# Kernel optimization log

Measured on AMD Instinct MI355X. Metric: run time of the kernel, lower is better.

## Reference

```python
import jax, jax.numpy as jnp
import numpy as np

EMBED_DIM = 1024
NUM_HEADS = 16
HEAD_DIM = EMBED_DIM // NUM_HEADS


def setup_inputs() -> dict:
    key = jax.random.key(0)
    ks = jax.random.split(key, 9)
    B, S, D = 4, 2048, EMBED_DIM
    s = 1.0 / np.sqrt(D)
    inp = {
        "x": jax.random.normal(ks[0], (B, S, D), dtype=jnp.float32),
        "Wq": jax.random.uniform(ks[1], (D, D), jnp.float32, -s, s),
        "bq": jax.random.uniform(ks[2], (D,), jnp.float32, -s, s),
        "Wk": jax.random.uniform(ks[3], (D, D), jnp.float32, -s, s),
        "bk": jax.random.uniform(ks[4], (D,), jnp.float32, -s, s),
        "Wv": jax.random.uniform(ks[5], (D, D), jnp.float32, -s, s),
        "bv": jax.random.uniform(ks[6], (D,), jnp.float32, -s, s),
        "Wo": jax.random.uniform(ks[7], (D, D), jnp.float32, -s, s),
        "bo": jax.random.uniform(ks[8], (D,), jnp.float32, -s, s),
    }
    return inp


def reference(x, Wq, bq, Wk, bk, Wv, bv, Wo, bo):
    B, S, D = x.shape
    H, Hd = NUM_HEADS, HEAD_DIM
    scale = 1.0 / jnp.sqrt(jnp.asarray(Hd, x.dtype))

    def split_heads(t):  # (B,S,D) -> (B,H,S,Hd)
        return t.reshape(B, S, H, Hd).transpose(0, 2, 1, 3)

    q = split_heads(x @ Wq + bq)
    k = split_heads(x @ Wk + bk)
    v = split_heads(x @ Wv + bv)

    scores = jnp.einsum("bhqd,bhkd->bhqk", q, k) * scale
    attn = jax.nn.softmax(scores, axis=-1)  # dropout is identity in eval mode
    out = jnp.einsum("bhqk,bhkd->bhqd", attn, v)
    out = out.transpose(0, 2, 1, 3).reshape(B, S, D)
    return out @ Wo + bo
```

## Files before the change

### kernel.cpp

```cpp
#include <hip/hip_runtime.h>
#include <cstdint>

typedef unsigned short u16;
typedef uint32_t u32;
typedef float f32x4 __attribute__((ext_vector_type(4)));
typedef short s16x8 __attribute__((ext_vector_type(8)));
typedef u16 u16x4 __attribute__((ext_vector_type(4)));
typedef u32 u32x2 __attribute__((ext_vector_type(2)));

__device__ __forceinline__ u16 f2bf(float f) {
  u32 u = __builtin_bit_cast(u32, f);
  u += 0x7FFFu + ((u >> 16) & 1u);
  return (u16)(u >> 16);
}

__device__ __forceinline__ u32 pack2bf(float lo, float hi) {
  return __builtin_amdgcn_perm(__builtin_bit_cast(u32, hi) + 0x8000u,
                               __builtin_bit_cast(u32, lo) + 0x8000u, 0x07060302u);
}

template <typename T>
__device__ __forceinline__ T ldv(const void* p) {
  T v;
  __builtin_memcpy(&v, __builtin_assume_aligned(p, 16), sizeof(T));
  return v;
}

__device__ __forceinline__ void gload_lds16(const void* g, void* l) {
  __builtin_amdgcn_global_load_lds((const __attribute__((address_space(1))) void*)g,
                                   (__attribute__((address_space(3))) void*)l, 16, 0, 0);
}

__global__ __launch_bounds__(256) void cvt_x_k(const float* __restrict__ in,
                                               u16* __restrict__ out) {
  const int i = (blockIdx.x * 256 + threadIdx.x) * 4;
  float4 v = *(const float4*)(in + i);
  u16x4 o;
  o.x = f2bf(v.x); o.y = f2bf(v.y); o.z = f2bf(v.z); o.w = f2bf(v.w);
  *(u16x4*)(out + i) = o;
}

__global__ __launch_bounds__(256) void prep_w_k(const float* __restrict__ Wq,
                                                const float* __restrict__ Wk,
                                                const float* __restrict__ Wv,
                                                const float* __restrict__ Wo,
                                                u16* __restrict__ out) {
  __shared__ u16 t[64][72];
  const float* W = (blockIdx.z == 0) ? Wq : (blockIdx.z == 1) ? Wk
                  : (blockIdx.z == 2) ? Wv : Wo;
  u16* O = out + (size_t)blockIdx.z * 1024 * 1024;
  const int n0 = blockIdx.x * 64, k0 = blockIdx.y * 64;
  const int tid = threadIdx.x;
#pragma unroll
  for (int i = 0; i < 16; ++i) {
    int e = i * 256 + tid;
    int r = e >> 6, c = e & 63;
    t[r][c] = f2bf(W[(size_t)(k0 + r) * 1024 + n0 + c]);
  }
  __syncthreads();
#pragma unroll
  for (int i = 0; i < 16; ++i) {
    int e = i * 256 + tid;
    int rr = e >> 6, cc = e & 63;
    O[(size_t)(n0 + rr) * 1024 + k0 + cc] = t[cc][rr];
  }
}

template <int MODE>
__global__ __launch_bounds__(256) void gemm_k(const u16* __restrict__ A,
                                              const u16* __restrict__ Bt,
                                              const float* __restrict__ bias,
                                              void* __restrict__ outp, float scale) {
  constexpr int K = 1024;
  __shared__ __attribute__((aligned(16))) u16 As[128][64];
  __shared__ __attribute__((aligned(16))) u16 Bs[128][64];
  const int tid = threadIdx.x;
  const int l = tid & 63, w = tid >> 6;
  const int lr = l & 15, lg = l >> 4;
  const int m0 = blockIdx.x * 128, n0 = blockIdx.y * 128;
  const int wr = (w >> 1) * 64, wc = (w & 1) * 64;
  const int rA = tid >> 3;
  const int cA = (tid & 7) * 8;

  f32x4 acc[4][4] = {};

  for (int kt = 0; kt < K; kt += 64) {
#pragma unroll
    for (int i = 0; i < 4; ++i) {
      gload_lds16(A + (size_t)(m0 + i * 32 + rA) * K + kt + cA,
                  &As[0][0] + (size_t)(i * 256 + w * 64) * 8);
      gload_lds16(Bt + (size_t)(n0 + i * 32 + rA) * K + kt + cA,
                  &Bs[0][0] + (size_t)(i * 256 + w * 64) * 8);
    }
    __syncthreads();
#pragma unroll
    for (int kk = 0; kk < 2; ++kk) {
      s16x8 a[4], b[4];
#pragma unroll
      for (int mi = 0; mi < 4; ++mi)
        a[mi] = ldv<s16x8>(&As[wr + mi * 16 + lr][kk * 32 + lg * 8]);
#pragma unroll
      for (int ni = 0; ni < 4; ++ni)
        b[ni] = ldv<s16x8>(&Bs[wc + ni * 16 + lr][kk * 32 + lg * 8]);
#pragma unroll
      for (int mi = 0; mi < 4; ++mi)
#pragma unroll
        for (int ni = 0; ni < 4; ++ni)
          acc[mi][ni] = __builtin_amdgcn_mfma_f32_16x16x32_bf16(a[mi], b[ni], acc[mi][ni], 0, 0, 0);
    }
    __syncthreads();
  }

#pragma unroll
  for (int ni = 0; ni < 4; ++ni) {
    const int col = n0 + wc + ni * 16 + lr;
    const float bv = bias[col];
#pragma unroll
    for (int mi = 0; mi < 4; ++mi) {
#pragma unroll
      for (int r = 0; r < 4; ++r) {
        const int rowm = m0 + wr + mi * 16 + lg * 4 + r;
        const float v = (acc[mi][ni][r] + bv) * scale;
        if constexpr (MODE == 2) {
          ((float*)outp)[(size_t)rowm * 1024 + col] = v;
        } else {
          const int bb = rowm >> 11, s = rowm & 2047;
          const int h = col >> 6, hd = col & 63;
          const u16 o = f2bf(v);
          if constexpr (MODE == 0) {
            ((u16*)outp)[((size_t)((bb << 4) + h) * 2048 + s) * 64 + hd] = o;
          } else if constexpr (MODE == 3) {
            const int hd_swz = ((((hd >> 3) ^ (s & 7)) & 7) << 3) | (hd & 7);
            ((u16*)outp)[((size_t)((bb << 4) + h) * 2048 + s) * 64 + hd_swz] = o;
          } else {
            const int s_swz = (s & ~63) | (((((s >> 3) & 7) ^ (hd & 7)) & 7) << 3) | (s & 7);
            ((u16*)outp)[((size_t)((bb << 4) + h) * 64 + hd) * 2048 + s_swz] = o;
          }
        }
      }
    }
  }
}

__global__ __launch_bounds__(512, 4) void attn_k(const u16* __restrict__ Qh,
                                                 const u16* __restrict__ Kg,
                                                 const u16* __restrict__ Vg,
                                                 u16* __restrict__ Oattn) {
  __shared__ __attribute__((aligned(16))) u16 Kbuf[2][4096];
  __shared__ __attribute__((aligned(16))) u16 Vbuf[2][4096];
  __shared__ __attribute__((aligned(16))) u16 P_lds[8][16][72];
  const int tid = threadIdx.x, l = tid & 63, w = tid >> 6;
  const int lr = l & 15, lg = l >> 4;
  const int bh = blockIdx.y;
  const int q0 = blockIdx.x * 256 + w * 32;
  const u16* Q = Qh + (size_t)bh * (2048 * 64);
  const u16* K = Kg + (size_t)bh * (2048 * 64);
  const u16* V = Vg + (size_t)bh * (64 * 2048);

  s16x8 qf[2][2];
#pragma unroll
  for (int f = 0; f < 2; ++f)
#pragma unroll
    for (int kk = 0; kk < 2; ++kk)
      qf[f][kk] = ldv<s16x8>(Q + (size_t)(q0 + f * 16 + lr) * 64 + kk * 32 + lg * 8);

  f32x4 acc[2][4] = {};
  float m_s[2] = {-1e30f, -1e30f}, l_s[2] = {0.f, 0.f};

#define STAGE(buf, kv0)                                                              \
  do {                                                                               \
    gload_lds16(K + (size_t)(kv0) * 64 + (size_t)tid * 8, &Kbuf[buf][w * 512]);      \
    gload_lds16(V + (size_t)(tid >> 3) * 2048 + (kv0) + (tid & 7) * 8,               \
                &Vbuf[buf][w * 512]);                                                \
  } while (0)

  STAGE(0, 0);
  __syncthreads();

  for (int t = 0; t < 32; ++t) {
    const int cur = t & 1;
    if (t < 31) STAGE(cur ^ 1, (t + 1) * 64);

    f32x4 s[2][4] = {};
#pragma unroll
    for (int tt = 0; tt < 4; ++tt) {
      s16x8 k0 = ldv<s16x8>(&Kbuf[cur][(tt * 16 + lr) * 64 + (((lg) ^ (lr & 7)) << 3)]);
      s16x8 k1 = ldv<s16x8>(&Kbuf[cur][(tt * 16 + lr) * 64 + (((4 + lg) ^ (lr & 7)) << 3)]);
#pragma unroll
      for (int f = 0; f < 2; ++f) {
        s[f][tt] = __builtin_amdgcn_mfma_f32_16x16x32_bf16(k0, qf[f][0], s[f][tt], 0, 0, 0);
        s[f][tt] = __builtin_amdgcn_mfma_f32_16x16x32_bf16(k1, qf[f][1], s[f][tt], 0, 0, 0);
      }
    }

    s16x8 pf[2][2];
#pragma unroll
    for (int f = 0; f < 2; ++f) {
      float a0 = fmaxf(fmaxf(s[f][0][0], s[f][0][1]), fmaxf(s[f][0][2], s[f][0][3]));
      float a1 = fmaxf(fmaxf(s[f][1][0], s[f][1][1]), fmaxf(s[f][1][2], s[f][1][3]));
      float a2 = fmaxf(fmaxf(s[f][2][0], s[f][2][1]), fmaxf(s[f][2][2], s[f][2][3]));
      float a3 = fmaxf(fmaxf(s[f][3][0], s[f][3][1]), fmaxf(s[f][3][2], s[f][3][3]));
      float pm = fmaxf(fmaxf(a0, a1), fmaxf(a2, a3));
      pm = fmaxf(pm, __shfl_xor(pm, 16));
      pm = fmaxf(pm, __shfl_xor(pm, 32));
      if (__any(pm > m_s[f] + 8.f)) {
        const float mnew = fmaxf(m_s[f], pm);
        const float alpha = __builtin_amdgcn_exp2f(m_s[f] - mnew);
        m_s[f] = mnew;
        l_s[f] *= alpha;
        float ar[4];
#pragma unroll
        for (int r = 0; r < 4; ++r) ar[r] = __shfl(alpha, lg * 4 + r);
#pragma unroll
        for (int dt = 0; dt < 4; ++dt)
#pragma unroll
          for (int r = 0; r < 4; ++r) acc[f][dt][r] *= ar[r];
      }
      const float mb = m_s[f];
#pragma unroll
      for (int tt = 0; tt < 4; ++tt)
#pragma unroll
        for (int r = 0; r < 4; ++r)
          s[f][tt][r] = __builtin_amdgcn_exp2f(s[f][tt][r] - mb);
      float b0 = (s[f][0][0] + s[f][0][1]) + (s[f][0][2] + s[f][0][3]);
      float b1 = (s[f][1][0] + s[f][1][1]) + (s[f][1][2] + s[f][1][3]);
      float b2 = (s[f][2][0] + s[f][2][1]) + (s[f][2][2] + s[f][2][3]);
      float b3 = (s[f][3][0] + s[f][3][1]) + (s[f][3][2] + s[f][3][3]);
      float ps = (b0 + b1) + (b2 + b3);
      ps += __shfl_xor(ps, 16);
      ps += __shfl_xor(ps, 32);
      l_s[f] += ps;
#pragma unroll
      for (int tt = 0; tt < 4; ++tt) {
        u32x2 pw;
        pw.x = pack2bf(s[f][tt][0], s[f][tt][1]);
        pw.y = pack2bf(s[f][tt][2], s[f][tt][3]);
        *(u32x2*)&P_lds[w][lr][tt * 16 + lg * 4] = pw;
      }
#pragma unroll
      for (int kvc = 0; kvc < 2; ++kvc)
        pf[f][kvc] = ldv<s16x8>(&P_lds[w][lr][kvc * 32 + lg * 8]);
    }

#pragma unroll
    for (int dt = 0; dt < 4; ++dt) {
      s16x8 v0 = ldv<s16x8>(&Vbuf[cur][(dt * 16 + lr) * 64 + (((lg) ^ (lr & 7)) << 3)]);
      s16x8 v1 = ldv<s16x8>(&Vbuf[cur][(dt * 16 + lr) * 64 + (((4 + lg) ^ (lr & 7)) << 3)]);
#pragma unroll
      for (int f = 0; f < 2; ++f) {
        acc[f][dt] = __builtin_amdgcn_mfma_f32_16x16x32_bf16(pf[f][0], v0, acc[f][dt], 0, 0, 0);
        acc[f][dt] = __builtin_amdgcn_mfma_f32_16x16x32_bf16(pf[f][1], v1, acc[f][dt], 0, 0, 0);
      }
    }
    __syncthreads();
  }
#undef STAGE

  const int b = bh >> 4, h = bh & 15;
#pragma unroll
  for (int f = 0; f < 2; ++f) {
    float li[4];
#pragma unroll
    for (int r = 0; r < 4; ++r) li[r] = 1.f / __shfl(l_s[f], lg * 4 + r);
#pragma unroll
    for (int dt = 0; dt < 4; ++dt)
#pragma unroll
      for (int r = 0; r < 4; ++r) {
        const int q = q0 + f * 16 + lg * 4 + r;
        Oattn[(size_t)((b << 11) + q) * 1024 + (h << 6) + dt * 16 + lr] =
            f2bf(acc[f][dt][r] * li[r]);
      }
  }
}

extern "C" void kernel_launch(void* const* d_in, const int* in_sizes, int n_in,
                              void* d_out, int out_size, void* d_ws, size_t ws_size,
                              hipStream_t stream) {
  const float* x  = (const float*)d_in[0];
  const float* Wq = (const float*)d_in[1];
  const float* bq = (const float*)d_in[2];
  const float* Wk = (const float*)d_in[3];
  const float* bk = (const float*)d_in[4];
  const float* Wv = (const float*)d_in[5];
  const float* bv = (const float*)d_in[6];
  const float* Wo = (const float*)d_in[7];
  const float* bo = (const float*)d_in[8];

  char* ws = (char*)d_ws;
  const size_t MB = 1u << 20;
  u16* xb = (u16*)(ws);
  u16* wt = (u16*)(ws + 16 * MB);
  u16* Qh = (u16*)(ws + 24 * MB);
  u16* Kh = (u16*)(ws + 40 * MB);
  u16* Vt = (u16*)(ws + 56 * MB);
  u16* attn = xb;

  const float qscale = 0.125f * 1.44269504088896f;

  cvt_x_k<<<dim3(8192), dim3(256), 0, stream>>>(x, xb);
  prep_w_k<<<dim3(16, 16, 4), dim3(256), 0, stream>>>(Wq, Wk, Wv, Wo, wt);
  gemm_k<0><<<dim3(64, 8), dim3(256), 0, stream>>>(xb, wt, bq, Qh, qscale);
  gemm_k<3><<<dim3(64, 8), dim3(256), 0, stream>>>(xb, wt + 1048576, bk, Kh, 1.0f);
  gemm_k<4><<<dim3(64, 8), dim3(256), 0, stream>>>(xb, wt + 2 * 1048576, bv, Vt, 1.0f);
  attn_k<<<dim3(8, 64), dim3(512), 0, stream>>>(Qh, Kh, Vt, attn);
  gemm_k<2><<<dim3(64, 8), dim3(256), 0, stream>>>(attn, wt + 3 * 1048576, bo, d_out, 1.0f);
}
```

Measured before the change: 228.1 us.

## Fuse QKV GEMMs into one launch and tune attention softmax bookkeeping

```diff
diff --git a/kernel.cpp b/kernel.cpp
--- a/kernel.cpp
+++ b/kernel.cpp
@@ -7,6 +7,7 @@
 typedef short s16x8 __attribute__((ext_vector_type(8)));
 typedef u16 u16x4 __attribute__((ext_vector_type(4)));
 typedef u32 u32x2 __attribute__((ext_vector_type(2)));
+typedef u32 u32x4 __attribute__((ext_vector_type(4)));
 
 __device__ __forceinline__ u16 f2bf(float f) {
   u32 u = __builtin_bit_cast(u32, f);
@@ -66,11 +67,94 @@
   }
 }
 
-template <int MODE>
-__global__ __launch_bounds__(256) void gemm_k(const u16* __restrict__ A,
-                                              const u16* __restrict__ Bt,
-                                              const float* __restrict__ bias,
-                                              void* __restrict__ outp, float scale) {
+__global__ __launch_bounds__(256) void gemm_qkv_k(const u16* __restrict__ A,
+                                                  const u16* __restrict__ Wt,
+                                                  const float* __restrict__ bq,
+                                                  const float* __restrict__ bk,
+                                                  const float* __restrict__ bv,
+                                                  u16* __restrict__ Qh,
+                                                  u16* __restrict__ Kh,
+                                                  u16* __restrict__ Vt,
+                                                  float qscale) {
+  constexpr int K = 1024;
+  __shared__ __attribute__((aligned(16))) u16 As[128][64];
+  __shared__ __attribute__((aligned(16))) u16 Bs[128][64];
+  const int tid = threadIdx.x;
+  const int l = tid & 63, w = tid >> 6;
+  const int lr = l & 15, lg = l >> 4;
+  const int m0 = blockIdx.x * 128;
+  const int ng = blockIdx.y * 128;
+  const int seg = ng >> 10;
+  const int n0 = ng & 1023;
+  const u16* Bt = Wt + ((size_t)seg << 20);
+  const int wr = (w >> 1) * 64, wc = (w & 1) * 64;
+  const int rA = tid >> 3;
+  const int cA = (tid & 7) * 8;
+
+  f32x4 acc[4][4] = {};
+
+  for (int kt = 0; kt < K; kt += 64) {
+#pragma unroll
+    for (int i = 0; i < 4; ++i) {
+      gload_lds16(A + (size_t)(m0 + i * 32 + rA) * K + kt + cA,
+                  &As[0][0] + (size_t)(i * 256 + w * 64) * 8);
+      gload_lds16(Bt + (size_t)(n0 + i * 32 + rA) * K + kt + cA,
+                  &Bs[0][0] + (size_t)(i * 256 + w * 64) * 8);
+    }
+    __syncthreads();
+#pragma unroll
+    for (int kk = 0; kk < 2; ++kk) {
+      s16x8 a[4], b[4];
+#pragma unroll
+      for (int mi = 0; mi < 4; ++mi)
+        a[mi] = ldv<s16x8>(&As[wr + mi * 16 + lr][kk * 32 + lg * 8]);
+#pragma unroll
+      for (int ni = 0; ni < 4; ++ni)
+        b[ni] = ldv<s16x8>(&Bs[wc + ni * 16 + lr][kk * 32 + lg * 8]);
+#pragma unroll
+      for (int mi = 0; mi < 4; ++mi)
+#pragma unroll
+        for (int ni = 0; ni < 4; ++ni)
+          acc[mi][ni] = __builtin_amdgcn_mfma_f32_16x16x32_bf16(a[mi], b[ni], acc[mi][ni], 0, 0, 0);
+    }
+    __syncthreads();
+  }
+
+  const float* bias = (seg == 0) ? bq : (seg == 1) ? bk : bv;
+  const float scale = (seg == 0) ? qscale : 1.0f;
+  u16* outp = (seg == 0) ? Qh : (seg == 1) ? Kh : Vt;
+
+#pragma unroll
+  for (int ni = 0; ni < 4; ++ni) {
+    const int col = n0 + wc + ni * 16 + lr;
+    const float bvv = bias[col];
+    const int h = col >> 6, hd = col & 63;
+#pragma unroll
+    for (int mi = 0; mi < 4; ++mi) {
+#pragma unroll
+      for (int r = 0; r < 4; ++r) {
+        const int rowm = m0 + wr + mi * 16 + lg * 4 + r;
+        const float v = (acc[mi][ni][r] + bvv) * scale;
+        const int bb = rowm >> 11, s = rowm & 2047;
+        const u16 o = f2bf(v);
+        if (seg == 0) {
+          outp[((size_t)((bb << 4) + h) * 2048 + s) * 64 + hd] = o;
+        } else if (seg == 1) {
+          const int hd_swz = ((((hd >> 3) ^ (s & 7)) & 7) << 3) | (hd & 7);
+          outp[((size_t)((bb << 4) + h) * 2048 + s) * 64 + hd_swz] = o;
+        } else {
+          const int s_swz = (s & ~63) | (((((s >> 3) & 7) ^ (hd & 7)) & 7) << 3) | (s & 7);
+          outp[((size_t)((bb << 4) + h) * 64 + hd) * 2048 + s_swz] = o;
+        }
+      }
+    }
+  }
+}
+
+__global__ __launch_bounds__(256) void gemm_o_k(const u16* __restrict__ A,
+                                                const u16* __restrict__ Bt,
+                                                const float* __restrict__ bias,
+                                                float* __restrict__ outp) {
   constexpr int K = 1024;
   __shared__ __attribute__((aligned(16))) u16 As[128][64];
   __shared__ __attribute__((aligned(16))) u16 Bs[128][64];
@@ -116,29 +200,12 @@
     const int col = n0 + wc + ni * 16 + lr;
     const float bv = bias[col];
 #pragma unroll
-    for (int mi = 0; mi < 4; ++mi) {
+    for (int mi = 0; mi < 4; ++mi)
 #pragma unroll
       for (int r = 0; r < 4; ++r) {
         const int rowm = m0 + wr + mi * 16 + lg * 4 + r;
-        const float v = (acc[mi][ni][r] + bv) * scale;
-        if constexpr (MODE == 2) {
-          ((float*)outp)[(size_t)rowm * 1024 + col] = v;
-        } else {
-          const int bb = rowm >> 11, s = rowm & 2047;
-          const int h = col >> 6, hd = col & 63;
-          const u16 o = f2bf(v);
-          if constexpr (MODE == 0) {
-            ((u16*)outp)[((size_t)((bb << 4) + h) * 2048 + s) * 64 + hd] = o;
-          } else if constexpr (MODE == 3) {
-            const int hd_swz = ((((hd >> 3) ^ (s & 7)) & 7) << 3) | (hd & 7);
-            ((u16*)outp)[((size_t)((bb << 4) + h) * 2048 + s) * 64 + hd_swz] = o;
-          } else {
-            const int s_swz = (s & ~63) | (((((s >> 3) & 7) ^ (hd & 7)) & 7) << 3) | (s & 7);
-            ((u16*)outp)[((size_t)((bb << 4) + h) * 64 + hd) * 2048 + s_swz] = o;
-          }
-        }
-      }
-    }
+        outp[(size_t)rowm * 1024 + col] = acc[mi][ni][r] + bv;
+      }
   }
 }
 
@@ -148,7 +215,7 @@
                                                  u16* __restrict__ Oattn) {
   __shared__ __attribute__((aligned(16))) u16 Kbuf[2][4096];
   __shared__ __attribute__((aligned(16))) u16 Vbuf[2][4096];
-  __shared__ __attribute__((aligned(16))) u16 P_lds[8][16][72];
+  __shared__ __attribute__((aligned(16))) u16 P_lds[8][16][64];
   const int tid = threadIdx.x, l = tid & 63, w = tid >> 6;
   const int lr = l & 15, lg = l >> 4;
   const int bh = blockIdx.y;
@@ -164,8 +231,12 @@
     for (int kk = 0; kk < 2; ++kk)
       qf[f][kk] = ldv<s16x8>(Q + (size_t)(q0 + f * 16 + lr) * 64 + kk * 32 + lg * 8);
 
+  const u32 one2 = 0x3F803F80u;
+  const s16x8 onesv = __builtin_bit_cast(s16x8, (u32x4){one2, one2, one2, one2});
+
   f32x4 acc[2][4] = {};
-  float m_s[2] = {-1e30f, -1e30f}, l_s[2] = {0.f, 0.f};
+  f32x4 lsum[2] = {};
+  float m_s[2] = {-1e30f, -1e30f};
 
 #define STAGE(buf, kv0)                                                              \
   do {                                                                               \
@@ -182,9 +253,10 @@
     if (t < 31) STAGE(cur ^ 1, (t + 1) * 64);
 
     f32x4 s[2][4] = {};
+    __builtin_amdgcn_s_setprio(1);
 #pragma unroll
     for (int tt = 0; tt < 4; ++tt) {
-      s16x8 k0 = ldv<s16x8>(&Kbuf[cur][(tt * 16 + lr) * 64 + (((lg) ^ (lr & 7)) << 3)]);
+      s16x8 k0 = ldv<s16x8>(&Kbuf[cur][(tt * 16 + lr) * 64 + ((lg ^ (lr & 7)) << 3)]);
       s16x8 k1 = ldv<s16x8>(&Kbuf[cur][(tt * 16 + lr) * 64 + (((4 + lg) ^ (lr & 7)) << 3)]);
 #pragma unroll
       for (int f = 0; f < 2; ++f) {
@@ -192,6 +264,7 @@
         s[f][tt] = __builtin_amdgcn_mfma_f32_16x16x32_bf16(k1, qf[f][1], s[f][tt], 0, 0, 0);
       }
     }
+    __builtin_amdgcn_s_setprio(0);
 
     s16x8 pf[2][2];
 #pragma unroll
@@ -201,13 +274,12 @@
       float a2 = fmaxf(fmaxf(s[f][2][0], s[f][2][1]), fmaxf(s[f][2][2], s[f][2][3]));
       float a3 = fmaxf(fmaxf(s[f][3][0], s[f][3][1]), fmaxf(s[f][3][2], s[f][3][3]));
       float pm = fmaxf(fmaxf(a0, a1), fmaxf(a2, a3));
-      pm = fmaxf(pm, __shfl_xor(pm, 16));
-      pm = fmaxf(pm, __shfl_xor(pm, 32));
       if (__any(pm > m_s[f] + 8.f)) {
+        pm = fmaxf(pm, __shfl_xor(pm, 16));
+        pm = fmaxf(pm, __shfl_xor(pm, 32));
         const float mnew = fmaxf(m_s[f], pm);
         const float alpha = __builtin_amdgcn_exp2f(m_s[f] - mnew);
         m_s[f] = mnew;
-        l_s[f] *= alpha;
         float ar[4];
 #pragma unroll
         for (int r = 0; r < 4; ++r) ar[r] = __shfl(alpha, lg * 4 + r);
@@ -215,6 +287,8 @@
         for (int dt = 0; dt < 4; ++dt)
 #pragma unroll
           for (int r = 0; r < 4; ++r) acc[f][dt][r] *= ar[r];
+#pragma unroll
+        for (int r = 0; r < 4; ++r) lsum[f][r] *= ar[r];
       }
       const float mb = m_s[f];
 #pragma unroll
@@ -222,29 +296,25 @@
 #pragma unroll
         for (int r = 0; r < 4; ++r)
           s[f][tt][r] = __builtin_amdgcn_exp2f(s[f][tt][r] - mb);
-      float b0 = (s[f][0][0] + s[f][0][1]) + (s[f][0][2] + s[f][0][3]);
-      float b1 = (s[f][1][0] + s[f][1][1]) + (s[f][1][2] + s[f][1][3]);
-      float b2 = (s[f][2][0] + s[f][2][1]) + (s[f][2][2] + s[f][2][3]);
-      float b3 = (s[f][3][0] + s[f][3][1]) + (s[f][3][2] + s[f][3][3]);
-      float ps = (b0 + b1) + (b2 + b3);
-      ps += __shfl_xor(ps, 16);
-      ps += __shfl_xor(ps, 32);
-      l_s[f] += ps;
 #pragma unroll
       for (int tt = 0; tt < 4; ++tt) {
         u32x2 pw;
         pw.x = pack2bf(s[f][tt][0], s[f][tt][1]);
         pw.y = pack2bf(s[f][tt][2], s[f][tt][3]);
-        *(u32x2*)&P_lds[w][lr][tt * 16 + lg * 4] = pw;
+        const int off = (((tt * 2 + (lg >> 1)) ^ (lr & 7)) << 3) + ((lg & 1) << 2);
+        *(u32x2*)&P_lds[w][lr][off] = pw;
       }
 #pragma unroll
       for (int kvc = 0; kvc < 2; ++kvc)
-        pf[f][kvc] = ldv<s16x8>(&P_lds[w][lr][kvc * 32 + lg * 8]);
-    }
-
+        pf[f][kvc] = ldv<s16x8>(&P_lds[w][lr][((kvc * 4 + lg) ^ (lr & 7)) << 3]);
+      lsum[f] = __builtin_amdgcn_mfma_f32_16x16x32_bf16(pf[f][0], onesv, lsum[f], 0, 0, 0);
+      lsum[f] = __builtin_amdgcn_mfma_f32_16x16x32_bf16(pf[f][1], onesv, lsum[f], 0, 0, 0);
+    }
+
+    __builtin_amdgcn_s_setprio(1);
 #pragma unroll
     for (int dt = 0; dt < 4; ++dt) {
-      s16x8 v0 = ldv<s16x8>(&Vbuf[cur][(dt * 16 + lr) * 64 + (((lg) ^ (lr & 7)) << 3)]);
+      s16x8 v0 = ldv<s16x8>(&Vbuf[cur][(dt * 16 + lr) * 64 + ((lg ^ (lr & 7)) << 3)]);
       s16x8 v1 = ldv<s16x8>(&Vbuf[cur][(dt * 16 + lr) * 64 + (((4 + lg) ^ (lr & 7)) << 3)]);
 #pragma unroll
       for (int f = 0; f < 2; ++f) {
@@ -252,6 +322,7 @@
         acc[f][dt] = __builtin_amdgcn_mfma_f32_16x16x32_bf16(pf[f][1], v1, acc[f][dt], 0, 0, 0);
       }
     }
+    __builtin_amdgcn_s_setprio(0);
     __syncthreads();
   }
 #undef STAGE
@@ -261,7 +332,7 @@
   for (int f = 0; f < 2; ++f) {
     float li[4];
 #pragma unroll
-    for (int r = 0; r < 4; ++r) li[r] = 1.f / __shfl(l_s[f], lg * 4 + r);
+    for (int r = 0; r < 4; ++r) li[r] = __builtin_amdgcn_rcpf(lsum[f][r]);
 #pragma unroll
     for (int dt = 0; dt < 4; ++dt)
 #pragma unroll
@@ -299,9 +370,7 @@
 
   cvt_x_k<<<dim3(8192), dim3(256), 0, stream>>>(x, xb);
   prep_w_k<<<dim3(16, 16, 4), dim3(256), 0, stream>>>(Wq, Wk, Wv, Wo, wt);
-  gemm_k<0><<<dim3(64, 8), dim3(256), 0, stream>>>(xb, wt, bq, Qh, qscale);
-  gemm_k<3><<<dim3(64, 8), dim3(256), 0, stream>>>(xb, wt + 1048576, bk, Kh, 1.0f);
-  gemm_k<4><<<dim3(64, 8), dim3(256), 0, stream>>>(xb, wt + 2 * 1048576, bv, Vt, 1.0f);
+  gemm_qkv_k<<<dim3(64, 24), dim3(256), 0, stream>>>(xb, wt, bq, bk, bv, Qh, Kh, Vt, qscale);
   attn_k<<<dim3(8, 64), dim3(512), 0, stream>>>(Qh, Kh, Vt, attn);
-  gemm_k<2><<<dim3(64, 8), dim3(256), 0, stream>>>(attn, wt + 3 * 1048576, bo, d_out, 1.0f);
-}
+  gemm_o_k<<<dim3(64, 8), dim3(256), 0, stream>>>(attn, wt + 3 * 1048576, bo, (float*)d_out);
+}
```

New measurement: 224.9 us. Within noise of the previous version (-1.4%).
